# Optimization experiments

Measured on AMD Instinct MI355X. Metric: run time of the kernel, lower is better.

The kernel has to match this reference:

```python
import jax, jax.numpy as jnp
import numpy as np

N_STEPS = 16
T_FINAL = 1.0


def setup_inputs() -> dict:
    key = jax.random.key(0)
    k = jax.random.split(key, 5)
    B, n, S = 131072, 8, 1
    return {
        "U0": jax.random.normal(k[0], (B, n, n), jnp.float32),
        "eps": jax.random.normal(k[1], (S, B, n, n), jnp.float32),
        "W0": 0.1 * jax.random.normal(k[2], (n, n), jnp.float32),
        "W1": 0.1 * jax.random.normal(k[3], (n, n), jnp.float32),
        "W2": 0.1 * jax.random.normal(k[4], (n, n), jnp.float32),
    }


def _alg_dyn(t, U, W0, W1, W2):
    # F(t, U; p) = antisym(W0 + t*W1 + U W2 U^T)  (real anti-Hermitian part)
    M = W0 + t * W1 + jnp.einsum('bij,jk,blk->bil', U, W2, U)
    return 0.5 * (M - jnp.swapaxes(M, -1, -2))


def _vel(t, U, W0, W1, W2):
    # dU/dt = F(t, U) @ U
    return _alg_dyn(t, U, W0, W1, W2) @ U


def _logj_rate(t, U, eps, W0, W1, W2):
    # Hutchinson estimator of tr(d vel / dU) per batch element: E_v[v . J v]
    f = lambda u: _vel(t, u, W0, W1, W2)

    def one(v):
        _, jv = jax.jvp(f, (U,), (v,))
        return jnp.sum(v * jv, axis=(-2, -1))  # [B]

    return jnp.mean(jax.vmap(one)(eps), axis=0)  # [B]


def reference(U0, eps, W0, W1, W2):
    dt = T_FINAL / N_STEPS

    def rhs(t, U):
        return _vel(t, U, W0, W1, W2), _logj_rate(t, U, eps, W0, W1, W2)

    def step(carry, i):
        U, lj = carry
        t = i.astype(U.dtype) * dt
        k1u, k1l = rhs(t, U)
        k2u, k2l = rhs(t + 0.5 * dt, U + 0.5 * dt * k1u)
        k3u, k3l = rhs(t + 0.5 * dt, U + 0.5 * dt * k2u)
        k4u, k4l = rhs(t + dt, U + dt * k3u)
        U = U + (dt / 6.0) * (k1u + 2.0 * k2u + 2.0 * k3u + k4u)
        lj = lj + (dt / 6.0) * (k1l + 2.0 * k2l + 2.0 * k3l + k4l)
        return (U, lj), None

    logj0 = jnp.zeros((U0.shape[0],), U0.dtype)
    (U, logj), _ = jax.lax.scan(step, (U0, logj0), jnp.arange(N_STEPS))
    return U, logj
```

## Files before the change

### kernel.cpp

```cpp
#include <hip/hip_runtime.h>
#include <stdint.h>

typedef unsigned int u32;
typedef unsigned short u16;

#define NSTEP 16
#define DTS (1.0f/16.0f)

#define TAB_FLAG 0
#define TAB_W2M  8
#define TAB_W2C  72
#define TAB_WT   112

typedef _Float16 f16;
typedef f16 h2 __attribute__((ext_vector_type(2)));

__device__ __forceinline__ float b2f(u16 h){ return __uint_as_float(((u32)h) << 16); }
__device__ __forceinline__ float bflo(u32 w){ return __uint_as_float(w << 16); }
__device__ __forceinline__ float bfhi(u32 w){ return __uint_as_float(w & 0xffff0000u); }
__device__ __forceinline__ u32 f2b(float f){
  u32 u = __float_as_uint(f);
  return (u + 0x7fffu + ((u >> 16) & 1u)) >> 16;
}
__host__ __device__ constexpr int TRI(int i, int j){ return i*7 - (i*(i-1))/2 + (j-i-1); }

__device__ __forceinline__ u32 pkh(float a, float b){
  return __builtin_bit_cast(u32, __builtin_amdgcn_cvt_pkrtz(a, b));
}
__device__ __forceinline__ h2 u2h(u32 x){ return __builtin_bit_cast(h2, x); }

__device__ __forceinline__ float dot8h(const u32* a, const u32* b){
  float s = __builtin_amdgcn_fdot2(u2h(a[0]), u2h(b[0]), 0.0f, false);
  s = __builtin_amdgcn_fdot2(u2h(a[1]), u2h(b[1]), s, false);
  s = __builtin_amdgcn_fdot2(u2h(a[2]), u2h(b[2]), s, false);
  s = __builtin_amdgcn_fdot2(u2h(a[3]), u2h(b[3]), s, false);
  return s;
}
__device__ __forceinline__ float Fel(const float* Fu, int i, int k){
  if (i == k) return 0.0f;
  return (i < k) ? Fu[TRI(i,k)] : -Fu[TRI(k,i)];
}

__global__ void prep_kernel(const void* __restrict__ W0v, const void* __restrict__ W1v,
                            const void* __restrict__ W2v, float* __restrict__ ws)
{
  __shared__ int sflag;
  __shared__ float sW0[64], sW1[64], sW2[64];
  int t = threadIdx.x;

  if (t == 0) {
    const u16* w2h = (const u16*)W2v;
    int ok = 1;
    for (int x = 0; x < 64; ++x) {
      float v = b2f(w2h[x]);
      if (!(v > -1024.0f && v < 1024.0f)) { ok = 0; break; }
    }
    sflag = ok;
    ws[TAB_FLAG] = (float)ok;
  }
  __syncthreads();
  int isbf = sflag;

  if (t < 64) {
    if (isbf) {
      sW0[t] = b2f(((const u16*)W0v)[t]);
      sW1[t] = b2f(((const u16*)W1v)[t]);
      sW2[t] = b2f(((const u16*)W2v)[t]);
    } else {
      sW0[t] = ((const float*)W0v)[t];
      sW1[t] = ((const float*)W1v)[t];
      sW2[t] = ((const float*)W2v)[t];
    }
  }
  __syncthreads();

  if (t < 64) {
    int i = t >> 3, j = t & 7;
    ws[TAB_W2M + t] = sW2[t] - sW2[j*8+i];
  }
  if (t < 32) {
    int j = t >> 2, kk = t & 3;
    ((u32*)ws)[TAB_W2C + t] = pkh(sW2[(2*kk)*8 + j], sW2[(2*kk+1)*8 + j]);
  }
  for (int idx = t; idx < 64*28; idx += 256) {
    int s = idx / 28;
    int e = idx - s*28;
    int i = 0, r = e;
    while (r >= 7 - i) { r -= 7 - i; ++i; }
    int j = i + 1 + r;
    int step = s >> 2, st = s & 3;
    float toff = (st == 0) ? 0.0f : ((st == 3) ? 1.0f : 0.5f);
    float tt = ((float)step + toff) * DTS;
    float w0a = 0.5f*(sW0[i*8+j] - sW0[j*8+i]);
    float w1a = 0.5f*(sW1[i*8+j] - sW1[j*8+i]);
    ws[TAB_WT + s*32 + e] = fmaf(tt, w1a, w0a);
  }
}

__global__ void __attribute__((amdgpu_flat_work_group_size(256,256), amdgpu_num_vgpr(256)))
flow_kernel(const void* __restrict__ U0v, const void* __restrict__ EPSv,
            const float* __restrict__ ws, void* __restrict__ outv, int B)
{
  __shared__ uint2 ve[256*32];
  const int tid = threadIdx.x;
  const int b = blockIdx.x * 256 + tid;
  uint2* myve = &ve[((tid >> 6) << 11) + (tid & 63)];
  if (b >= B) return;
  const int isbf = (ws[TAB_FLAG] != 0.0f);

  float Us[64];

  {
    float V[64];
    if (isbf) {
      const uint4* pu = (const uint4*)((const u16*)U0v + (size_t)b*64);
      const uint4* pv = (const uint4*)((const u16*)EPSv + (size_t)b*64);
      #pragma unroll
      for (int q = 0; q < 8; ++q) {
        uint4 xu = pu[q];
        uint4 xv = pv[q];
        Us[8*q+0]=bflo(xu.x); Us[8*q+1]=bfhi(xu.x);
        Us[8*q+2]=bflo(xu.y); Us[8*q+3]=bfhi(xu.y);
        Us[8*q+4]=bflo(xu.z); Us[8*q+5]=bfhi(xu.z);
        Us[8*q+6]=bflo(xu.w); Us[8*q+7]=bfhi(xu.w);
        V[8*q+0]=bflo(xv.x); V[8*q+1]=bfhi(xv.x);
        V[8*q+2]=bflo(xv.y); V[8*q+3]=bfhi(xv.y);
        V[8*q+4]=bflo(xv.z); V[8*q+5]=bfhi(xv.z);
        V[8*q+6]=bflo(xv.w); V[8*q+7]=bfhi(xv.w);
      }
    } else {
      const float4* pu = (const float4*)((const float*)U0v + (size_t)b*64);
      const float4* pv = (const float4*)((const float*)EPSv + (size_t)b*64);
      #pragma unroll
      for (int q = 0; q < 16; ++q) {
        float4 xu = pu[q];
        float4 xv = pv[q];
        Us[4*q+0]=xu.x; Us[4*q+1]=xu.y; Us[4*q+2]=xu.z; Us[4*q+3]=xu.w;
        V[4*q+0]=xv.x; V[4*q+1]=xv.y; V[4*q+2]=xv.z; V[4*q+3]=xv.w;
      }
    }
    const float* M = ws + TAB_W2M;
    #pragma unroll
    for (int i = 0; i < 8; ++i) {
      float e[8];
      #pragma unroll
      for (int j = 0; j < 8; ++j) {
        float s = V[i*8+0] * M[0*8+j];
        #pragma unroll
        for (int k = 1; k < 8; ++k) s = fmaf(V[i*8+k], M[k*8+j], s);
        e[j] = s;
      }
      myve[(2*i+0)*64]  = make_uint2(pkh(V[i*8+0],V[i*8+1]), pkh(V[i*8+2],V[i*8+3]));
      myve[(2*i+1)*64]  = make_uint2(pkh(V[i*8+4],V[i*8+5]), pkh(V[i*8+6],V[i*8+7]));
      myve[(16+2*i)*64] = make_uint2(pkh(e[0],e[1]), pkh(e[2],e[3]));
      myve[(17+2*i)*64] = make_uint2(pkh(e[4],e[5]), pkh(e[6],e[7]));
    }
  }

  u32 w2c[32];
  #pragma unroll
  for (int x = 0; x < 32; ++x) w2c[x] = ((const u32*)ws)[TAB_W2C + x];

  float lj = 0.0f;

  #pragma unroll 1
  for (int step = 0; step < NSTEP; ++step) {
    float acc[64];
    u32 Uh[32];
    #pragma unroll
    for (int x = 0; x < 32; ++x) {
      Uh[x] = pkh(Us[2*x], Us[2*x+1]);
      acc[2*x] = 0.0f; acc[2*x+1] = 0.0f;
    }

    #pragma unroll 1
    for (int stage = 0; stage < 4; ++stage) {
      const float* wt = ws + TAB_WT + (size_t)(((step << 2) | stage) << 5);

      float D[28];
      #pragma unroll
      for (int r = 0; r < 8; ++r) {
        uint2 va = myve[(2*r+0)*64];
        uint2 vb = myve[(2*r+1)*64];
        u32 vr[4] = {va.x, va.y, vb.x, vb.y};
        #pragma unroll
        for (int m = 0; m < 8; ++m) {
          if (m == r) continue;
          float dv = dot8h(vr, Uh + m*4);
          if (m > r) D[TRI(r,m)] = dv;
          else       D[TRI(m,r)] -= dv;
        }
      }
      float Ssum = 0.0f;
      #pragma unroll
      for (int r = 0; r < 8; ++r) {
        uint2 ea = myve[(16+2*r)*64];
        uint2 eb = myve[(17+2*r)*64];
        u32 er[4] = {ea.x, ea.y, eb.x, eb.y};
        #pragma unroll
        for (int m = 0; m < 8; ++m) {
          if (m == r) continue;
          float de = dot8h(er, Uh + m*4);
          Ssum = fmaf(de, (m > r) ? D[TRI(r,m)] : -D[TRI(m,r)], Ssum);
        }
      }
      float cl = (stage == 1 || stage == 2) ? (DTS/6.0f) : (DTS/12.0f);
      lj = fmaf(cl, Ssum, lj);

      float Fu[28];
      #pragma unroll
      for (int r = 0; r < 8; ++r) {
        float ar[8];
        #pragma unroll
        for (int j = 0; j < 8; ++j) ar[j] = dot8h(Uh + r*4, w2c + j*4);
        u32 Ah[4];
        #pragma unroll
        for (int kk = 0; kk < 4; ++kk) Ah[kk] = pkh(ar[2*kk], ar[2*kk+1]);
        #pragma unroll
        for (int j = 0; j < 8; ++j) {
          if (j == r) continue;
          float da = dot8h(Ah, Uh + j*4);
          if (j > r) Fu[TRI(r,j)] = fmaf(0.5f, da, wt[TRI(r,j)]);
          else       Fu[TRI(j,r)] = fmaf(-0.5f, da, Fu[TRI(j,r)]);
        }
      }

      u32 Fh[32];
      #pragma unroll
      for (int i = 0; i < 8; ++i)
        #pragma unroll
        for (int kk = 0; kk < 4; ++kk)
          Fh[i*4+kk] = pkh(Fel(Fu, i, 2*kk), Fel(Fu, i, 2*kk+1));

      u32 Uc[32];
      #pragma unroll
      for (int kk = 0; kk < 4; ++kk) {
        #pragma unroll
        for (int jh = 0; jh < 4; ++jh) {
          u32 A  = Uh[(2*kk)*4 + jh];
          u32 Bv = Uh[(2*kk+1)*4 + jh];
          Uc[(2*jh+0)*4 + kk] = (A & 0xffffu) | (Bv << 16);
          Uc[(2*jh+1)*4 + kk] = (A >> 16) | (Bv & 0xffff0000u);
        }
      }

      float wa = (stage == 1 || stage == 2) ? 2.0f : 1.0f;
      float cs = (stage == 2) ? DTS : (0.5f*DTS);
      #pragma unroll
      for (int i = 0; i < 8; ++i) {
        #pragma unroll
        for (int jh = 0; jh < 4; ++jh) {
          float kva = dot8h(Fh + i*4, Uc + (2*jh+0)*4);
          float kvb = dot8h(Fh + i*4, Uc + (2*jh+1)*4);
          acc[i*8+2*jh+0] = fmaf(wa, kva, acc[i*8+2*jh+0]);
          acc[i*8+2*jh+1] = fmaf(wa, kvb, acc[i*8+2*jh+1]);
          if (stage < 3)
            Uh[i*4+jh] = pkh(fmaf(cs, kva, Us[i*8+2*jh+0]),
                             fmaf(cs, kvb, Us[i*8+2*jh+1]));
        }
      }
    }
    #pragma unroll
    for (int x = 0; x < 64; ++x) Us[x] = fmaf(DTS/6.0f, acc[x], Us[x]);
  }

  if (isbf) {
    u16* outU = (u16*)outv;
    uint4* po = (uint4*)(outU + (size_t)b*64);
    #pragma unroll
    for (int q = 0; q < 8; ++q) {
      uint4 o;
      o.x = f2b(Us[8*q+0]) | (f2b(Us[8*q+1]) << 16);
      o.y = f2b(Us[8*q+2]) | (f2b(Us[8*q+3]) << 16);
      o.z = f2b(Us[8*q+4]) | (f2b(Us[8*q+5]) << 16);
      o.w = f2b(Us[8*q+6]) | (f2b(Us[8*q+7]) << 16);
      po[q] = o;
    }
    outU[(size_t)B*64 + b] = (u16)f2b(lj);
  } else {
    float* outU = (float*)outv;
    float4* po = (float4*)(outU + (size_t)b*64);
    #pragma unroll
    for (int q = 0; q < 16; ++q) {
      po[q] = make_float4(Us[4*q+0], Us[4*q+1], Us[4*q+2], Us[4*q+3]);
    }
    outU[(size_t)B*64 + b] = lj;
  }
}

extern "C" void kernel_launch(void* const* d_in, const int* in_sizes, int n_in,
                              void* d_out, int out_size, void* d_ws, size_t ws_size,
                              hipStream_t stream) {
  const void* U0  = d_in[0];
  const void* EPS = d_in[1];
  const void* W0  = d_in[2];
  const void* W1  = d_in[3];
  const void* W2  = d_in[4];
  float* ws = (float*)d_ws;
  int B = in_sizes[0] / 64;

  hipLaunchKernelGGL(prep_kernel, dim3(1), dim3(256), 0, stream, W0, W1, W2, ws);
  hipLaunchKernelGGL(flow_kernel, dim3((B + 255) / 256), dim3(256), 0, stream,
                     U0, EPS, ws, d_out, B);
}
```

Baseline: 618.9 us.

## Fuse Hutchinson dot passes antisymmetrically, double-buffer LDS reads, shrink transposed-U registers

The two passes over the probe rows (v and eps) are merged into one. For each off-diagonal pair, the trace term is now the product of two antisymmetric differences, so the v-side matrix no longer has to be fully built before the eps pass starts. LDS reads of the probe rows are double-buffered in groups of four, so the next group loads while the current one is computed. The column-transposed copy of U is now built one column pair at a time instead of as a full 32-register array, and the kernel is pinned to 2 waves per EU. Together these aim to cut register pressure and LDS latency stalls, at the cost of a different fp rounding order in the log-det sum.

```diff
diff --git a/kernel.cpp b/kernel.cpp
--- a/kernel.cpp
+++ b/kernel.cpp
@@ -97,7 +97,8 @@
   }
 }
 
-__global__ void __attribute__((amdgpu_flat_work_group_size(256,256), amdgpu_num_vgpr(256)))
+__global__ void __attribute__((amdgpu_flat_work_group_size(256,256),
+                               amdgpu_waves_per_eu(2,2), amdgpu_num_vgpr(256)))
 flow_kernel(const void* __restrict__ U0v, const void* __restrict__ EPSv,
             const float* __restrict__ ws, void* __restrict__ outv, int B)
 {
@@ -177,31 +178,38 @@
     for (int stage = 0; stage < 4; ++stage) {
       const float* wt = ws + TAB_WT + (size_t)(((step << 2) | stage) << 5);
 
-      float D[28];
-      #pragma unroll
-      for (int r = 0; r < 8; ++r) {
-        uint2 va = myve[(2*r+0)*64];
-        uint2 vb = myve[(2*r+1)*64];
-        u32 vr[4] = {va.x, va.y, vb.x, vb.y};
-        #pragma unroll
-        for (int m = 0; m < 8; ++m) {
-          if (m == r) continue;
-          float dv = dot8h(vr, Uh + m*4);
-          if (m > r) D[TRI(r,m)] = dv;
-          else       D[TRI(m,r)] -= dv;
-        }
-      }
+      float Dv[28], De[28];
       float Ssum = 0.0f;
-      #pragma unroll
-      for (int r = 0; r < 8; ++r) {
-        uint2 ea = myve[(16+2*r)*64];
-        uint2 eb = myve[(17+2*r)*64];
-        u32 er[4] = {ea.x, ea.y, eb.x, eb.y};
-        #pragma unroll
-        for (int m = 0; m < 8; ++m) {
-          if (m == r) continue;
-          float de = dot8h(er, Uh + m*4);
-          Ssum = fmaf(de, (m > r) ? D[TRI(r,m)] : -D[TRI(m,r)], Ssum);
+      {
+        uint2 bA[8], bB[8];
+        #pragma unroll
+        for (int q = 0; q < 4; ++q) bA[q]   = myve[(0  + q)*64];
+        #pragma unroll
+        for (int q = 0; q < 4; ++q) bA[4+q] = myve[(16 + q)*64];
+        #pragma unroll
+        for (int g = 0; g < 4; ++g) {
+          const uint2* cur = (g & 1) ? bB : bA;
+          uint2*       nxt = (g & 1) ? bA : bB;
+          if (g < 3) {
+            #pragma unroll
+            for (int q = 0; q < 4; ++q) nxt[q]   = myve[(4*(g+1)      + q)*64];
+            #pragma unroll
+            for (int q = 0; q < 4; ++q) nxt[4+q] = myve[(16 + 4*(g+1) + q)*64];
+          }
+          #pragma unroll
+          for (int rr = 0; rr < 2; ++rr) {
+            const int r = 2*g + rr;
+            u32 vr[4] = {cur[2*rr].x, cur[2*rr].y, cur[2*rr+1].x, cur[2*rr+1].y};
+            u32 er[4] = {cur[4+2*rr].x, cur[4+2*rr].y, cur[4+2*rr+1].x, cur[4+2*rr+1].y};
+            #pragma unroll
+            for (int m = 0; m < 8; ++m) {
+              if (m == r) continue;
+              float dv = dot8h(vr, Uh + m*4);
+              float de = dot8h(er, Uh + m*4);
+              if (m > r) { Dv[TRI(r,m)] = dv; De[TRI(r,m)] = de; }
+              else       Ssum = fmaf(Dv[TRI(m,r)] - dv, De[TRI(m,r)] - de, Ssum);
+            }
+          }
         }
       }
       float cl = (stage == 1 || stage == 2) ? (DTS/6.0f) : (DTS/12.0f);
@@ -232,26 +240,22 @@
         for (int kk = 0; kk < 4; ++kk)
           Fh[i*4+kk] = pkh(Fel(Fu, i, 2*kk), Fel(Fu, i, 2*kk+1));
 
-      u32 Uc[32];
-      #pragma unroll
-      for (int kk = 0; kk < 4; ++kk) {
-        #pragma unroll
-        for (int jh = 0; jh < 4; ++jh) {
+      float wa = (stage == 1 || stage == 2) ? 2.0f : 1.0f;
+      float cs = (stage == 2) ? DTS : (0.5f*DTS);
+      #pragma unroll
+      for (int jh = 0; jh < 4; ++jh) {
+        u32 c0[4], c1[4];
+        #pragma unroll
+        for (int kk = 0; kk < 4; ++kk) {
           u32 A  = Uh[(2*kk)*4 + jh];
           u32 Bv = Uh[(2*kk+1)*4 + jh];
-          Uc[(2*jh+0)*4 + kk] = (A & 0xffffu) | (Bv << 16);
-          Uc[(2*jh+1)*4 + kk] = (A >> 16) | (Bv & 0xffff0000u);
+          c0[kk] = (A & 0xffffu) | (Bv << 16);
+          c1[kk] = (A >> 16) | (Bv & 0xffff0000u);
         }
-      }
-
-      float wa = (stage == 1 || stage == 2) ? 2.0f : 1.0f;
-      float cs = (stage == 2) ? DTS : (0.5f*DTS);
-      #pragma unroll
-      for (int i = 0; i < 8; ++i) {
-        #pragma unroll
-        for (int jh = 0; jh < 4; ++jh) {
-          float kva = dot8h(Fh + i*4, Uc + (2*jh+0)*4);
-          float kvb = dot8h(Fh + i*4, Uc + (2*jh+1)*4);
+        #pragma unroll
+        for (int i = 0; i < 8; ++i) {
+          float kva = dot8h(Fh + i*4, c0);
+          float kvb = dot8h(Fh + i*4, c1);
           acc[i*8+2*jh+0] = fmaf(wa, kva, acc[i*8+2*jh+0]);
           acc[i*8+2*jh+1] = fmaf(wa, kvb, acc[i*8+2*jh+1]);
           if (stage < 3)
```

New measurement: 1.028 ms. 66.1% more time.
